# Optimization experiments

Measured on AMD Instinct MI355X. Metric: run time of the kernel, lower is better.

The kernel has to match this reference:

```python
import jax, jax.numpy as jnp
import numpy as np

COMMIT_WEIGHT = 0.25


def setup_inputs() -> dict:
    key = jax.random.key(0)
    k1, k2 = jax.random.split(key)
    B, D, T, K = 8, 512, 2048, 8192
    x = jax.random.normal(k1, (B, D, T), dtype=jnp.float32)
    codebook = jax.random.normal(k2, (K, D), dtype=jnp.float32)
    return {"x": x, "codebook": codebook}


def reference(x, codebook):
    # x: [B, D, T] channels-first; VQ operates on [B, T, D]
    xt = jnp.transpose(x, (0, 2, 1))  # [B, T, D]
    x2 = jnp.sum(xt * xt, axis=-1, keepdims=True)          # [B, T, 1]
    e2 = jnp.sum(codebook * codebook, axis=-1)             # [K]
    xe = jnp.einsum('btd,kd->btk', xt, codebook)           # [B, T, K] (dominant GEMM)
    dists = x2 - 2.0 * xe + e2                             # [B, T, K]
    indices = jnp.argmin(dists, axis=-1)                   # [B, T] int
    quantized = codebook[indices]                          # [B, T, D] gather
    # commitment loss: ||sg(q) - x||^2 mean
    commit_loss = COMMIT_WEIGHT * jnp.mean(
        (jax.lax.stop_gradient(quantized) - xt) ** 2)
    # straight-through estimator
    quantized = xt + jax.lax.stop_gradient(quantized - xt)
    quantized = jnp.transpose(quantized, (0, 2, 1))        # back to [B, D, T]
    return quantized, indices, commit_loss
```

## Files before the change

kernel.cpp:

```cpp
#include <hip/hip_runtime.h>
#include <cstdint>
#include <cstddef>

#define B_   8
#define D_   512
#define T_   2048
#define K_   8192
#define BT_  (B_ * T_)
#define NQ_  ((size_t)B_ * D_ * T_)

typedef _Float16 f16x8 __attribute__((ext_vector_type(8)));
typedef _Float16 f16x4 __attribute__((ext_vector_type(4)));
typedef float    f32x4 __attribute__((ext_vector_type(4)));
typedef unsigned long long u64;
typedef unsigned int u32;

#define WS_SLOTS_OFF    0
#define WS_FIDX_OFF     393216
#define WS_PART_OFF     458752
#define WS_E2_OFF       460800
#define WS_XH_OFF       524288
#define WS_XL_OFF       (WS_XH_OFF + 16777216)
#define WS_CH_OFF       (WS_XL_OFF + 16777216)
#define WS_NEEDED       ((size_t)WS_CH_OFF + 8388608)

__device__ __forceinline__ void gload_lds16(const void* g, void* l) {
    __builtin_amdgcn_global_load_lds(
        (const __attribute__((address_space(1))) void*)g,
        (__attribute__((address_space(3))) void*)l, 16, 0, 0);
}

__device__ __forceinline__ u32 fkey(float f) {
    u32 u = __float_as_uint(f);
    u ^= (u32)((int)u >> 31) | 0x80000000u;
    return u;
}
__device__ __forceinline__ u64 umin64(u64 a, u64 b) { return a < b ? a : b; }
__device__ __forceinline__ u64 umax64(u64 a, u64 b) { return a > b ? a : b; }

__global__ __launch_bounds__(256) void k_e2(const float* __restrict__ cb,
                                            float* __restrict__ e2) {
    int k = blockIdx.x * 256 + threadIdx.x;
    const float4* row = (const float4*)(cb + (size_t)k * D_);
    float s = 0.f;
#pragma unroll 4
    for (int i = 0; i < D_ / 4; ++i) {
        float4 v = row[i];
        s = fmaf(v.x, v.x, s); s = fmaf(v.y, v.y, s);
        s = fmaf(v.z, v.z, s); s = fmaf(v.w, v.w, s);
    }
    e2[k] = s;
}

__global__ __launch_bounds__(256) void k_splitcb(const float* __restrict__ cb,
                                                 _Float16* __restrict__ ch) {
    size_t i = ((size_t)blockIdx.x * 256 + threadIdx.x) * 4;
    float4 v = *(const float4*)(cb + i);
    f16x4 h;
    h[0] = (_Float16)v.x; h[1] = (_Float16)v.y;
    h[2] = (_Float16)v.z; h[3] = (_Float16)v.w;
    *(f16x4*)(ch + i) = h;
}

__global__ __launch_bounds__(256) void k_splitx(const float* __restrict__ x,
                                                _Float16* __restrict__ xh,
                                                _Float16* __restrict__ xl) {
    int b  = blockIdx.z;
    int d0 = blockIdx.y * 64;
    int t0 = blockIdx.x * 64;
    int dl = threadIdx.x & 63;
    int tq = threadIdx.x >> 6;
    const float* px = x + ((size_t)b * D_ + (d0 + dl)) * T_ + t0;
#pragma unroll 4
    for (int i = 0; i < 16; ++i) {
        int t = tq * 16 + i;
        float v = px[t];
        _Float16 h = (_Float16)v;
        float lo = v - (float)h;
        _Float16 l = (_Float16)lo;
        size_t row = (size_t)b * T_ + t0 + t;
        xh[row * D_ + d0 + dl] = h;
        xl[row * D_ + d0 + dl] = l;
    }
}

__global__ __launch_bounds__(512, 2)
void k_hi_argmin(const _Float16* __restrict__ xh, const _Float16* __restrict__ ch,
                 const float* __restrict__ e2, u64* __restrict__ slots) {
    __shared__ char smem[131072];
    __shared__ u32 stop[256][2][2];
    __shared__ float e2s[1024];

    const int tid = threadIdx.x;
    const int xcd = blockIdx.x & 7;
    const int bi  = blockIdx.x >> 3;
    const int m_  = bi >> 3;
    const int nblk = bi & 7;
    const int mbase  = (xcd * 8 + m_) * 256;
    const int nstart = nblk * 1024;

    const int lane = tid & 63;
    const int wid  = tid >> 6;
    const int wr = wid & 3, wc = wid >> 2;
    const int lr = lane & 15, lg = lane >> 4;

    {
        u32* p = (u32*)stop;
        p[tid] = ~0u; p[tid + 512] = ~0u;
        *(float2*)&e2s[tid * 2] = *(const float2*)&e2[nstart + tid * 2];
    }
    __syncthreads();

    const bool isA = wid < 4;
    const int srow8 = lane >> 3;
    const int sswz = ((lane & 7) ^ srow8) * 16;
    const char* gs0 = isA
        ? (const char*)xh + (size_t)(mbase  + (wid & 3) * 64 + srow8) * 1024 + sswz
        : (const char*)ch + (size_t)(nstart + (wid & 3) * 64 + srow8) * 1024 + sswz;
    const int ldsbase = (isA ? 0 : 32768) + (wid & 3) * 8192;

#define STAGEQ(bufi, g, i0, cnt) do {                                        \
        char* lb_ = smem + (bufi) * 65536 + ldsbase;                         \
        const char* gs_ = gs0 + (isA ? 0 : (size_t)((g) >> 3) * 262144)      \
                          + ((g) & 7) * 128;                                 \
        _Pragma("unroll")                                                    \
        for (int i_ = (i0); i_ < (i0) + (cnt); ++i_)                         \
            gload_lds16(gs_ + (size_t)i_ * 8192, lb_ + i_ * 1024);           \
    } while (0)

    const int s7 = lr & 7;
    const int aoff0 = (wr * 64 + lr) * 128 + ((lg ^ s7) * 16);
    const int boff0 = 32768 + (wc * 128 + lr) * 128 + ((lg ^ s7) * 16);

    u32 top2a[16], top2b[16];
#pragma unroll
    for (int s = 0; s < 16; ++s) { top2a[s] = ~0u; top2b[s] = ~0u; }

    f32x4 acc[4][8];
#pragma unroll
    for (int m = 0; m < 4; ++m)
#pragma unroll
        for (int n = 0; n < 8; ++n)
            acc[m][n] = (f32x4){0.f, 0.f, 0.f, 0.f};

    auto epilogue = [&](int ns) {
        float e2v[8];
#pragma unroll
        for (int n = 0; n < 8; ++n)
            e2v[n] = 0.5f * e2s[ns * 256 + wc * 128 + n * 16 + lr];
        const u32 base10 = ((u32)ns << 8) | ((u32)wc << 7) | (u32)lr;
#pragma unroll
        for (int m = 0; m < 4; ++m) {
#pragma unroll
            for (int j = 0; j < 4; ++j) {
                const int s = m * 4 + j;
                u32 t1 = top2a[s], t2 = top2b[s];
#pragma unroll
                for (int n = 0; n < 8; ++n) {
                    float d = fmaxf(e2v[n] - acc[m][n][j], 1.0f);
                    u32 p = (__float_as_uint(d) & 0xFFFFFC00u) | (base10 + ((u32)n << 4));
                    u32 mx = t1 > p ? t1 : p;
                    t1 = t1 < p ? t1 : p;
                    t2 = t2 < mx ? t2 : mx;
                }
                top2a[s] = t1; top2b[s] = t2;
            }
        }
#pragma unroll
        for (int m = 0; m < 4; ++m)
#pragma unroll
            for (int n = 0; n < 8; ++n)
                acc[m][n] = (f32x4){0.f, 0.f, 0.f, 0.f};
    };

#define MFMA16(AF, BF, NOFF)                                                 \
        __builtin_amdgcn_s_setprio(1);                                       \
        _Pragma("unroll")                                                    \
        for (int m = 0; m < 4; ++m)                                          \
            _Pragma("unroll")                                                \
            for (int n = 0; n < 4; ++n)                                      \
                acc[m][(NOFF) + n] = __builtin_amdgcn_mfma_f32_16x16x32_f16( \
                    AF[m], BF[n], acc[m][(NOFF) + n], 0, 0, 0);              \
        __builtin_amdgcn_s_setprio(0);

#define SB __builtin_amdgcn_sched_barrier(0)

    STAGEQ(0, 0, 0, 8);
    asm volatile("s_waitcnt vmcnt(0)" ::: "memory");
    __builtin_amdgcn_s_barrier();
    int cur = 0;

#pragma unroll 1
    for (int t = 0; t < 32; ++t) {
        const char* base = smem + cur * 65536;
        f16x8 afA[4], afB[4], bfA[4], bfB[4], bfC[4], bfD[4];

#pragma unroll
        for (int m = 0; m < 4; ++m)
            afA[m] = *(const f16x8*)(base + aoff0 + m * 2048);
#pragma unroll
        for (int n = 0; n < 4; ++n)
            bfA[n] = *(const f16x8*)(base + boff0 + n * 2048);
        if (t < 31) STAGEQ(cur ^ 1, t + 1, 0, 4);
        SB;
#pragma unroll
        for (int n = 0; n < 4; ++n)
            bfB[n] = *(const f16x8*)(base + boff0 + (4 + n) * 2048);
        if (t < 31) STAGEQ(cur ^ 1, t + 1, 4, 2);
        SB;
        MFMA16(afA, bfA, 0)
        SB;
#pragma unroll
        for (int m = 0; m < 4; ++m)
            afB[m] = *(const f16x8*)(base + (aoff0 ^ 64) + m * 2048);
#pragma unroll
        for (int n = 0; n < 4; ++n)
            bfC[n] = *(const f16x8*)(base + (boff0 ^ 64) + n * 2048);
        if (t < 31) STAGEQ(cur ^ 1, t + 1, 6, 2);
        SB;
        MFMA16(afA, bfB, 4)
        SB;
#pragma unroll
        for (int n = 0; n < 4; ++n)
            bfD[n] = *(const f16x8*)(base + (boff0 ^ 64) + (4 + n) * 2048);
        SB;
        MFMA16(afB, bfC, 0)
        SB;
        MFMA16(afB, bfD, 4)
        SB;

        asm volatile("s_waitcnt vmcnt(0)" ::: "memory");
        SB;
        __builtin_amdgcn_s_barrier();
        cur ^= 1;
        if ((t & 7) == 7) epilogue(t >> 3);
    }
#undef STAGEQ
#undef MFMA16
#undef SB

#pragma unroll
    for (int m = 0; m < 4; ++m) {
#pragma unroll
        for (int j = 0; j < 4; ++j) {
            const int s = m * 4 + j;
            u32 t1 = top2a[s], t2 = top2b[s];
#pragma unroll
            for (int st = 1; st < 16; st <<= 1) {
                u32 o1 = __shfl_xor(t1, st);
                u32 o2 = __shfl_xor(t2, st);
                u32 mx = t1 > o1 ? t1 : o1;
                u32 sel = t1 < o1 ? t2 : o2;
                u32 n2 = mx < sel ? mx : sel;
                t1 = t1 < o1 ? t1 : o1;
                t2 = t2 < n2 ? t2 : n2;
            }
            if (lr == 0) {
                int ql = wr * 64 + m * 16 + lg * 4 + j;
                stop[ql][wc][0] = t1; stop[ql][wc][1] = t2;
            }
        }
    }

    __syncthreads();
    if (tid < 256) {
        u32 a1 = stop[tid][0][0], a2 = stop[tid][0][1];
        u32 b1 = stop[tid][1][0], b2 = stop[tid][1][1];
        u32 f1 = a1 < b1 ? a1 : b1;
        u32 mx = a1 > b1 ? a1 : b1;
        u32 sel = a1 < b1 ? a2 : b2;
        u32 f2 = mx < sel ? mx : sel;
        int q = mbase + tid;
        u64 p1 = ((u64)(f1 & 0xFFFFFC00u) << 32) | (u32)(nstart + (f1 & 0x3FFu));
        u64 p2 = ((u64)(f2 & 0xFFFFFC00u) << 32) | (u32)(nstart + (f2 & 0x3FFu));
        u64* As = slots + q;
        u64* Bs = slots + BT_ + q;
        u64* Cs = slots + 2 * BT_ + q;
        u64 old = atomicMin(As, p1);
        u64 v = umax64(old, p1);
        old = atomicMin(Bs, v);
        u64 v2 = umax64(old, v);
        atomicMin(Cs, v2);
        old = atomicMin(Bs, p2);
        v = umax64(old, p2);
        atomicMin(Cs, v);
    }
}

__global__ __launch_bounds__(256)
void k_rescore(const _Float16* __restrict__ xh, const _Float16* __restrict__ xl,
               const float* __restrict__ cb, const float* __restrict__ e2,
               const u64* __restrict__ slots,
               u32* __restrict__ final_idx, float* __restrict__ out_idx) {
    const int wid = threadIdx.x >> 6, lane = threadIdx.x & 63;
    const int q = blockIdx.x * 4 + wid;
    u64 a = slots[q], b = slots[BT_ + q], c = slots[2 * BT_ + q];
    u32 i1 = (u32)a, i2 = (u32)b, i3 = (u32)c;
    float d1 = __uint_as_float((u32)(a >> 32));
    float d2 = __uint_as_float((u32)(b >> 32));
    u32 win = i1;
    if (!(d2 - d1 > 0.75f)) {
        float xr[8];
        f16x8 hv = *(const f16x8*)(xh + (size_t)q * D_ + lane * 8);
        f16x8 lv = *(const f16x8*)(xl + (size_t)q * D_ + lane * 8);
#pragma unroll
        for (int i = 0; i < 8; ++i) xr[i] = (float)hv[i] + (float)lv[i];
        u32 idxs[3] = {i1, i2, i3};
        float key[3];
#pragma unroll 1
        for (int cnd = 0; cnd < 3; ++cnd) {
            const float4* cr = (const float4*)(cb + (size_t)idxs[cnd] * D_ + lane * 8);
            float4 c0 = cr[0], c1 = cr[1];
            float s = xr[0] * c0.x;
            s = fmaf(xr[1], c0.y, s); s = fmaf(xr[2], c0.z, s); s = fmaf(xr[3], c0.w, s);
            s = fmaf(xr[4], c1.x, s); s = fmaf(xr[5], c1.y, s);
            s = fmaf(xr[6], c1.z, s); s = fmaf(xr[7], c1.w, s);
#pragma unroll
            for (int st = 1; st < 64; st <<= 1) s += __shfl_xor(s, st);
            key[cnd] = e2[idxs[cnd]] - 2.f * s;
        }
        float bk = key[0]; win = idxs[0];
#pragma unroll
        for (int cnd = 1; cnd < 3; ++cnd) {
            if (key[cnd] < bk || (key[cnd] == bk && idxs[cnd] < win)) {
                bk = key[cnd]; win = idxs[cnd];
            }
        }
    }
    if (lane == 0) { final_idx[q] = win; out_idx[q] = (float)win; }
}

#define MB 64
#define NB 64
#define KC 32
#define FNSPLIT 2
#define KPER (K_ / FNSPLIT)
__global__ __launch_bounds__(256, 2)
void k_argmin_f32(const float* __restrict__ x, const float* __restrict__ cb,
                  const float* __restrict__ e2, u64* __restrict__ slots) {
    __shared__ float xs[KC][MB + 4];
    __shared__ float es[KC][NB + 4];
    __shared__ u64 red[MB];
    const int tid = threadIdx.x;
    const int tx = tid & 15, ty = tid >> 4;
    const int rowtile = blockIdx.x;
    const int b = rowtile >> 5;
    const int tbase = (rowtile & 31) * MB;
    const int nstart = blockIdx.y * KPER;
    if (tid < MB) red[tid] = ~0ull;
    float bestv[4]; int besti[4];
#pragma unroll
    for (int i = 0; i < 4; ++i) { bestv[i] = 3.4e38f; besti[i] = 0; }
    const int sm = tid & 63, sg = tid >> 6;
    const float* xbase = x + (size_t)b * D_ * T_ + (tbase + sm);
    for (int nb = 0; nb < KPER; nb += NB) {
        float acc[4][4];
#pragma unroll
        for (int i = 0; i < 4; ++i)
#pragma unroll
            for (int j = 0; j < 4; ++j) acc[i][j] = 0.f;
        for (int kc = 0; kc < D_; kc += KC) {
            __syncthreads();
#pragma unroll
            for (int r = 0; r < 8; ++r) {
                int dd = sg * 8 + r;
                xs[dd][sm] = xbase[(size_t)(kc + dd) * T_];
            }
            const float* crow = cb + (size_t)(nstart + nb + sm) * D_ + kc + sg * 8;
            float4 c0 = *(const float4*)(crow);
            float4 c1 = *(const float4*)(crow + 4);
            es[sg * 8 + 0][sm] = c0.x; es[sg * 8 + 1][sm] = c0.y;
            es[sg * 8 + 2][sm] = c0.z; es[sg * 8 + 3][sm] = c0.w;
            es[sg * 8 + 4][sm] = c1.x; es[sg * 8 + 5][sm] = c1.y;
            es[sg * 8 + 6][sm] = c1.z; es[sg * 8 + 7][sm] = c1.w;
            __syncthreads();
#pragma unroll
            for (int dd = 0; dd < KC; ++dd) {
                float4 a = *(const float4*)&xs[dd][tx * 4];
                float4 e = *(const float4*)&es[dd][ty * 4];
                acc[0][0] = fmaf(a.x, e.x, acc[0][0]); acc[0][1] = fmaf(a.x, e.y, acc[0][1]);
                acc[0][2] = fmaf(a.x, e.z, acc[0][2]); acc[0][3] = fmaf(a.x, e.w, acc[0][3]);
                acc[1][0] = fmaf(a.y, e.x, acc[1][0]); acc[1][1] = fmaf(a.y, e.y, acc[1][1]);
                acc[1][2] = fmaf(a.y, e.z, acc[1][2]); acc[1][3] = fmaf(a.y, e.w, acc[1][3]);
                acc[2][0] = fmaf(a.z, e.x, acc[2][0]); acc[2][1] = fmaf(a.z, e.y, acc[2][1]);
                acc[2][2] = fmaf(a.z, e.z, acc[2][2]); acc[2][3] = fmaf(a.z, e.w, acc[2][3]);
                acc[3][0] = fmaf(a.w, e.x, acc[3][0]); acc[3][1] = fmaf(a.w, e.y, acc[3][1]);
                acc[3][2] = fmaf(a.w, e.z, acc[3][2]); acc[3][3] = fmaf(a.w, e.w, acc[3][3]);
            }
        }
#pragma unroll
        for (int j = 0; j < 4; ++j) {
            int c = nstart + nb + ty * 4 + j;
            float ec = e2[c];
#pragma unroll
            for (int i = 0; i < 4; ++i) {
                float dist = fmaf(-2.f, acc[i][j], ec);
                if (dist < bestv[i]) { bestv[i] = dist; besti[i] = c; }
            }
        }
    }
    __syncthreads();
#pragma unroll
    for (int i = 0; i < 4; ++i) {
        u64 p = ((u64)fkey(bestv[i]) << 32) | (u32)besti[i];
        atomicMin(&red[tx * 4 + i], p);
    }
    __syncthreads();
    if (tid < MB) atomicMin(&slots[b * T_ + tbase + tid], red[tid]);
}

__global__ __launch_bounds__(256)
void k_finalize(const u64* __restrict__ slots,
                u32* __restrict__ final_idx, float* __restrict__ out_idx) {
    int q = blockIdx.x * 256 + threadIdx.x;
    u32 idx = (u32)slots[q];
    final_idx[q] = idx;
    out_idx[q] = (float)idx;
}

__global__ __launch_bounds__(256)
void k_gather(const float* __restrict__ x, const float* __restrict__ cb,
              const u32* __restrict__ final_idx,
              float* __restrict__ out_q, float* __restrict__ partials) {
    int tid = threadIdx.x;
    int btg = blockIdx.x * 256 + tid;
    int b = btg >> 11, t = btg & (T_ - 1);
    int dch = blockIdx.y;
    u32 idx = final_idx[btg];
    const float* crow = cb + (size_t)idx * D_;
    size_t xoff = (size_t)b * D_ * T_ + t;
    float ls = 0.f;
#pragma unroll 4
    for (int dd = 0; dd < 64; ++dd) {
        int d = dch * 64 + dd;
        float q = crow[d];
        size_t o = xoff + (size_t)d * T_;
        float xv = x[o];
        out_q[o] = q;
        float df = q - xv;
        ls = fmaf(df, df, ls);
    }
    __shared__ float rs[256];
    rs[tid] = ls;
    __syncthreads();
    for (int s = 128; s > 0; s >>= 1) {
        if (tid < s) rs[tid] += rs[tid + s];
        __syncthreads();
    }
    if (tid == 0) partials[blockIdx.y * 64 + blockIdx.x] = rs[0];
}

__global__ __launch_bounds__(256)
void k_loss(const float* __restrict__ partials, float* __restrict__ out_loss) {
    __shared__ float rs[256];
    int tid = threadIdx.x;
    float s = partials[tid] + partials[tid + 256];
    rs[tid] = s;
    __syncthreads();
    for (int st = 128; st > 0; st >>= 1) {
        if (tid < st) rs[tid] += rs[tid + st];
        __syncthreads();
    }
    if (tid == 0) out_loss[0] = 0.25f * rs[0] / (float)NQ_;
}

extern "C" void kernel_launch(void* const* d_in, const int* in_sizes, int n_in,
                              void* d_out, int out_size, void* d_ws, size_t ws_size,
                              hipStream_t stream) {
    const float* x  = (const float*)d_in[0];
    const float* cb = (const float*)d_in[1];

    float* out_q    = (float*)d_out;
    float* out_idx  = out_q + NQ_;
    float* out_loss = out_idx + BT_;

    char* ws = (char*)d_ws;
    u64* slots = (u64*)(ws + WS_SLOTS_OFF);
    u32* fidx = (u32*)(ws + WS_FIDX_OFF);
    float* partials = (float*)(ws + WS_PART_OFF);
    float* e2 = (float*)(ws + WS_E2_OFF);

    hipMemsetAsync(slots, 0xFF, (size_t)3 * BT_ * 8, stream);
    k_e2<<<dim3(K_ / 256), dim3(256), 0, stream>>>(cb, e2);

    if (ws_size >= WS_NEEDED) {
        _Float16* xhp = (_Float16*)(ws + WS_XH_OFF);
        _Float16* xlp = (_Float16*)(ws + WS_XL_OFF);
        _Float16* chp = (_Float16*)(ws + WS_CH_OFF);
        k_splitcb<<<dim3((K_ * D_ / 4) / 256), dim3(256), 0, stream>>>(cb, chp);
        k_splitx<<<dim3(T_ / 64, D_ / 64, B_), dim3(256), 0, stream>>>(x, xhp, xlp);
        k_hi_argmin<<<dim3(512), dim3(512), 0, stream>>>(xhp, chp, e2, slots);
        k_rescore<<<dim3(BT_ / 4), dim3(256), 0, stream>>>(xhp, xlp, cb, e2, slots,
                                                           fidx, out_idx);
    } else {
        k_argmin_f32<<<dim3(BT_ / MB, FNSPLIT), dim3(256), 0, stream>>>(x, cb, e2, slots);
        k_finalize<<<dim3(BT_ / 256), dim3(256), 0, stream>>>(slots, fidx, out_idx);
    }

    k_gather<<<dim3(BT_ / 256, D_ / 64), dim3(256), 0, stream>>>(x, cb, fidx,
                                                                 out_q, partials);
    k_loss<<<dim3(1), dim3(256), 0, stream>>>(partials, out_loss);
}
```

Baseline: 217.8 us.

## Switch GEMM main loop to 4-stage ring buffer with smaller K-steps

Replaces the double-buffered 128-byte K-step pipeline with a 4-slot LDS ring of 64-byte K-steps. Global-to-LDS loads are issued three stages ahead and waited on with a partial vmcnt, so more loads stay in flight across barriers. It also drops the XOR swizzle on the LDS layout, which may bring back LDS bank conflicts on the fragment reads. The loop now runs 64 iterations and hits a barrier on each one, twice as many as before.

```diff
diff --git a/kernel.cpp b/kernel.cpp
--- a/kernel.cpp
+++ b/kernel.cpp
@@ -112,25 +112,23 @@
     __syncthreads();
 
     const bool isA = wid < 4;
-    const int srow8 = lane >> 3;
-    const int sswz = ((lane & 7) ^ srow8) * 16;
     const char* gs0 = isA
-        ? (const char*)xh + (size_t)(mbase  + (wid & 3) * 64 + srow8) * 1024 + sswz
-        : (const char*)ch + (size_t)(nstart + (wid & 3) * 64 + srow8) * 1024 + sswz;
-    const int ldsbase = (isA ? 0 : 32768) + (wid & 3) * 8192;
-
-#define STAGEQ(bufi, g, i0, cnt) do {                                        \
-        char* lb_ = smem + (bufi) * 65536 + ldsbase;                         \
-        const char* gs_ = gs0 + (isA ? 0 : (size_t)((g) >> 3) * 262144)      \
-                          + ((g) & 7) * 128;                                 \
-        _Pragma("unroll")                                                    \
-        for (int i_ = (i0); i_ < (i0) + (cnt); ++i_)                         \
-            gload_lds16(gs_ + (size_t)i_ * 8192, lb_ + i_ * 1024);           \
+        ? (const char*)xh + (size_t)(mbase  + (wid & 3) * 64 + (lane >> 2)) * 1024
+              + (lane & 3) * 16
+        : (const char*)ch + (size_t)(nstart + (wid & 3) * 64 + (lane >> 2)) * 1024
+              + (lane & 3) * 16;
+    const int ldsbase = (isA ? 0 : 16384) + (wid & 3) * 4096;
+
+#define STAGE2(g, i0) do {                                                   \
+        char* lb_ = smem + ((g) & 3) * 32768 + ldsbase;                      \
+        const char* gs_ = gs0 + (isA ? 0 : (size_t)((g) >> 4) * 262144)      \
+                          + ((g) & 15) * 64;                                 \
+        gload_lds16(gs_ + (size_t)(i0) * 16384, lb_ + (i0) * 1024);          \
+        gload_lds16(gs_ + (size_t)((i0) + 1) * 16384, lb_ + ((i0) + 1) * 1024); \
     } while (0)
 
-    const int s7 = lr & 7;
-    const int aoff0 = (wr * 64 + lr) * 128 + ((lg ^ s7) * 16);
-    const int boff0 = 32768 + (wc * 128 + lr) * 128 + ((lg ^ s7) * 16);
+    const int aoff0 = (wr * 64 + lr) * 64 + lg * 16;
+    const int boff0 = 16384 + (wc * 128 + lr) * 64 + lg * 16;
 
     u32 top2a[16], top2b[16];
 #pragma unroll
@@ -185,57 +183,46 @@
 
 #define SB __builtin_amdgcn_sched_barrier(0)
 
-    STAGEQ(0, 0, 0, 8);
-    asm volatile("s_waitcnt vmcnt(0)" ::: "memory");
+    STAGE2(0, 0); STAGE2(0, 2);
+    STAGE2(1, 0); STAGE2(1, 2);
+    STAGE2(2, 0); STAGE2(2, 2);
+    asm volatile("s_waitcnt vmcnt(8)" ::: "memory");
     __builtin_amdgcn_s_barrier();
-    int cur = 0;
+    SB;
 
 #pragma unroll 1
-    for (int t = 0; t < 32; ++t) {
-        const char* base = smem + cur * 65536;
-        f16x8 afA[4], afB[4], bfA[4], bfB[4], bfC[4], bfD[4];
+    for (int s = 0; s < 64; ++s) {
+        const char* base = smem + (s & 3) * 32768;
+        f16x8 af[4], bf[4], bg[4];
 
 #pragma unroll
         for (int m = 0; m < 4; ++m)
-            afA[m] = *(const f16x8*)(base + aoff0 + m * 2048);
+            af[m] = *(const f16x8*)(base + aoff0 + m * 1024);
 #pragma unroll
         for (int n = 0; n < 4; ++n)
-            bfA[n] = *(const f16x8*)(base + boff0 + n * 2048);
-        if (t < 31) STAGEQ(cur ^ 1, t + 1, 0, 4);
+            bf[n] = *(const f16x8*)(base + boff0 + n * 1024);
+        if (s < 61) STAGE2(s + 3, 0);
+        SB;
+        MFMA16(af, bf, 0)
         SB;
 #pragma unroll
         for (int n = 0; n < 4; ++n)
-            bfB[n] = *(const f16x8*)(base + boff0 + (4 + n) * 2048);
-        if (t < 31) STAGEQ(cur ^ 1, t + 1, 4, 2);
-        SB;
-        MFMA16(afA, bfA, 0)
-        SB;
-#pragma unroll
-        for (int m = 0; m < 4; ++m)
-            afB[m] = *(const f16x8*)(base + (aoff0 ^ 64) + m * 2048);
-#pragma unroll
-        for (int n = 0; n < 4; ++n)
-            bfC[n] = *(const f16x8*)(base + (boff0 ^ 64) + n * 2048);
-        if (t < 31) STAGEQ(cur ^ 1, t + 1, 6, 2);
-        SB;
-        MFMA16(afA, bfB, 4)
-        SB;
-#pragma unroll
-        for (int n = 0; n < 4; ++n)
-            bfD[n] = *(const f16x8*)(base + (boff0 ^ 64) + (4 + n) * 2048);
-        SB;
-        MFMA16(afB, bfC, 0)
-        SB;
-        MFMA16(afB, bfD, 4)
-        SB;
-
-        asm volatile("s_waitcnt vmcnt(0)" ::: "memory");
+            bg[n] = *(const f16x8*)(base + boff0 + (4 + n) * 1024);
+        if (s < 61) STAGE2(s + 3, 2);
+        SB;
+        MFMA16(af, bg, 4)
+        SB;
+
+        if (s < 61)       asm volatile("s_waitcnt vmcnt(8)" ::: "memory");
+        else if (s == 61) asm volatile("s_waitcnt vmcnt(4)" ::: "memory");
+        else              asm volatile("s_waitcnt vmcnt(0)" ::: "memory");
+        asm volatile("s_waitcnt lgkmcnt(0)" ::: "memory");
         SB;
         __builtin_amdgcn_s_barrier();
-        cur ^= 1;
-        if ((t & 7) == 7) epilogue(t >> 3);
-    }
-#undef STAGEQ
+        SB;
+        if ((s & 15) == 15) epilogue(s >> 4);
+    }
+#undef STAGE2
 #undef MFMA16
 #undef SB
 
```

Result: slower. 223.7 us (+2.7%).
